# Kernel optimization log

Hardware: AMD Instinct MI355X
Metric: run time of the kernel (lower is better)

Reference implementation:

```python
import jax, jax.numpy as jnp
import numpy as np
from functools import partial

B, T, F, H = 32768, 48, 16, 32  # batch, horizon, feature dim, rnn_size


def setup_inputs() -> dict:
    key = jax.random.key(0)
    ks = jax.random.split(key, 9)
    return {
        "decoder_feature": jax.random.normal(ks[0], (B, T, F), dtype=jnp.float32),
        "decoder_init_input": jax.random.normal(ks[1], (B, 1), dtype=jnp.float32),
        "init_state": jax.random.normal(ks[2], (B, H), dtype=jnp.float32),
        # GRUCell (Keras default reset_after=True): kernel [in_dim, 3H], recurrent [H, 3H], two biases
        "kernel": jax.random.normal(ks[3], (1 + F, 3 * H), dtype=jnp.float32) * 0.1,
        "recurrent_kernel": jax.random.normal(ks[4], (H, 3 * H), dtype=jnp.float32) * 0.1,
        "bias_x": jax.random.normal(ks[5], (3 * H,), dtype=jnp.float32) * 0.1,
        "bias_h": jax.random.normal(ks[6], (3 * H,), dtype=jnp.float32) * 0.1,
        "dense_w": jax.random.normal(ks[7], (H, 1), dtype=jnp.float32) * 0.1,
        "dense_b": jax.random.normal(ks[8], (1,), dtype=jnp.float32) * 0.1,
    }


def reference(decoder_feature, decoder_init_input, init_state,
              kernel, recurrent_kernel, bias_x, bias_h, dense_w, dense_b):
    units = init_state.shape[-1]

    def step(carry, feat_t):
        h, prev_out = carry                              # h: [B,H], prev_out: [B,1]
        x = jnp.concatenate([prev_out, feat_t], axis=1)  # [B, 1+F]
        mx = x @ kernel + bias_x                         # [B, 3H]
        mh = h @ recurrent_kernel + bias_h               # [B, 3H] (reset_after=True)
        xz, xr, xh = jnp.split(mx, 3, axis=1)
        hz, hr, hh_in = jnp.split(mh, 3, axis=1)
        z = jax.nn.sigmoid(xz + hz)
        r = jax.nn.sigmoid(xr + hr)
        hh = jnp.tanh(xh + r * hh_in)
        h_new = z * h + (1.0 - z) * hh                   # GRU output == new state
        out = h_new @ dense_w + dense_b                  # Dense(1): [B,1]
        return (h_new, out), out

    feats = jnp.transpose(decoder_feature, (1, 0, 2))    # [T,B,F] time-major for scan
    _, outs = jax.lax.scan(step, (init_state, decoder_init_input), feats)
    return jnp.transpose(outs, (1, 0, 2))                # [B,T,1]
```

## Files before the change

kernel.cpp:

```cpp
#include <hip/hip_runtime.h>


typedef __attribute__((ext_vector_type(8))) short short8;
typedef __attribute__((ext_vector_type(4))) float f32x4;

constexpr int T_STEPS = 48;
constexpr int F_DIM   = 16;
constexpr int H_DIM   = 32;
constexpr int ROW_SH  = 40;
constexpr int H_BYTES = 16 * ROW_SH * 2;
constexpr int O_FLOATS = 16 * T_STEPS;
constexpr int WAVE_BYTES = H_BYTES + O_FLOATS * 4;

union S8 { short8 s; unsigned u[4]; };

__device__ __forceinline__ unsigned pk_bf16(float hi, float lo) {
    return __builtin_amdgcn_perm(__float_as_uint(hi) + 0x8000u,
                                 __float_as_uint(lo) + 0x8000u, 0x07060302u);
}
__device__ __forceinline__ short bf16s(float x) {
    return (short)((__float_as_uint(x) + 0x8000u) >> 16);
}
__device__ __forceinline__ float fsig(float x) {
    return __builtin_amdgcn_rcpf(1.0f + __expf(-x));
}
__device__ __forceinline__ float ftanh(float x) {
    return 1.0f - 2.0f * __builtin_amdgcn_rcpf(__expf(2.0f * x) + 1.0f);
}
#define MFMA(a, b, c) __builtin_amdgcn_mfma_f32_16x16x32_bf16(a, b, c, 0, 0, 0)
#define SWZ16(v) __int_as_float(__builtin_amdgcn_ds_swizzle(__float_as_int(v), 0x401F))

__global__ __launch_bounds__(256, 2)
void gru_mfma4(const float* __restrict__ feat,
               const float* __restrict__ init_in,
               const float* __restrict__ init_h,
               const float* __restrict__ Wk,
               const float* __restrict__ Rk,
               const float* __restrict__ bx,
               const float* __restrict__ bh,
               const float* __restrict__ dw,
               const float* __restrict__ db,
               float* __restrict__ out)
{
    __shared__ __align__(16) char lds[4 * WAVE_BYTES];
    const int lane = threadIdx.x & 63;
    const int wave = threadIdx.x >> 6;
    const int ln   = lane & 15;
    const int quad = lane >> 4;
    const int b0   = (blockIdx.x * 4 + wave) * 16;

    char*  my   = lds + wave * WAVE_BYTES;
    short* hsh  = (short*)my;
    float* obuf = (float*)(my + H_BYTES);
    unsigned* hw = (unsigned*)(hsh + ln * ROW_SH + quad * 4);
    const short8* hr = (const short8*)(hsh + ln * ROW_SH + quad * 8);
    const int bpa = (lane ^ 32) << 2;

    S8 Wf[6], Rf[6];
#pragma unroll
    for (int tn = 0; tn < 6; ++tn) {
#pragma unroll
        for (int j = 0; j < 8; ++j) {
            const int k = quad * 8 + j;
            const int n = tn * 16 + ln;
            const float wv = (k < 16) ? Wk[(size_t)(k + 1) * 96 + n] : 0.0f;
            Wf[tn].s[j] = bf16s(wv);
            Rf[tn].s[j] = bf16s(Rk[(size_t)k * 96 + n]);
        }
    }

    float bz8[8], br8[8], bxh8[8], bhh8[8], wz8[8], wr8[8], wh8[8], dw8[8];
#pragma unroll
    for (int tn = 0; tn < 2; ++tn)
#pragma unroll
        for (int i = 0; i < 4; ++i) {
            const int c = tn * 16 + quad * 4 + i;
            const int idx = tn * 4 + i;
            bz8[idx]  = bx[c] + bh[c];
            br8[idx]  = bx[32 + c] + bh[32 + c];
            bxh8[idx] = bx[64 + c];
            bhh8[idx] = bh[64 + c];
            wz8[idx]  = Wk[c];
            wr8[idx]  = Wk[32 + c];
            wh8[idx]  = Wk[64 + c];
            dw8[idx]  = dw[c];
        }
    const float dbs = db[0];

    float hc[8];
#pragma unroll
    for (int tn = 0; tn < 2; ++tn)
#pragma unroll
        for (int i = 0; i < 4; ++i)
            hc[tn * 4 + i] = init_h[(size_t)(b0 + ln) * H_DIM + tn * 16 + quad * 4 + i];
    S8 hB;
    {
        const float* hp = init_h + (size_t)(b0 + ln) * H_DIM + quad * 8;
        const f32x4 a = *(const f32x4*)hp;
        const f32x4 b = *(const f32x4*)(hp + 4);
        hB.u[0] = pk_bf16(a[1], a[0]); hB.u[1] = pk_bf16(a[3], a[2]);
        hB.u[2] = pk_bf16(b[1], b[0]); hB.u[3] = pk_bf16(b[3], b[2]);
    }
    float po = init_in[b0 + ln];

    const float* fqb = feat + (size_t)(b0 + ln) * (T_STEPS * F_DIM) + (quad & 1) * 8;
    f32x4 pa = *(const f32x4*)(fqb);
    f32x4 pb = *(const f32x4*)(fqb + 4);

    for (int t = 0; t < T_STEPS; ++t) {
        S8 xa;
        xa.u[0] = pk_bf16(pa[1], pa[0]); xa.u[1] = pk_bf16(pa[3], pa[2]);
        xa.u[2] = pk_bf16(pb[1], pb[0]); xa.u[3] = pk_bf16(pb[3], pb[2]);
        const unsigned zm = (quad < 2) ? 0xFFFFFFFFu : 0u;
        xa.u[0] &= zm; xa.u[1] &= zm; xa.u[2] &= zm; xa.u[3] &= zm;

        const int t1 = (t < T_STEPS - 1) ? t + 1 : T_STEPS - 1;
        pa = *(const f32x4*)(fqb + t1 * F_DIM);
        pb = *(const f32x4*)(fqb + t1 * F_DIM + 4);

        f32x4 aZ[2], aR[2], aXH[2], aHH[2];
#pragma unroll
        for (int tn = 0; tn < 2; ++tn)
#pragma unroll
            for (int i = 0; i < 4; ++i) {
                const int idx = tn * 4 + i;
                aZ[tn][i]  = fmaf(po, wz8[idx], bz8[idx]);
                aR[tn][i]  = fmaf(po, wr8[idx], br8[idx]);
                aXH[tn][i] = fmaf(po, wh8[idx], bxh8[idx]);
                aHH[tn][i] = bhh8[idx];
            }
#pragma unroll
        for (int tn = 0; tn < 2; ++tn) {
            aZ[tn]  = MFMA(Wf[tn].s,     xa.s, aZ[tn]);
            aZ[tn]  = MFMA(Rf[tn].s,     hB.s, aZ[tn]);
            aR[tn]  = MFMA(Wf[2 + tn].s, xa.s, aR[tn]);
            aR[tn]  = MFMA(Rf[2 + tn].s, hB.s, aR[tn]);
            aXH[tn] = MFMA(Wf[4 + tn].s, xa.s, aXH[tn]);
            aHH[tn] = MFMA(Rf[4 + tn].s, hB.s, aHH[tn]);
        }

        float hn[8];
        float partial = 0.0f;
#pragma unroll
        for (int tn = 0; tn < 2; ++tn)
#pragma unroll
            for (int i = 0; i < 4; ++i) {
                const int idx = tn * 4 + i;
                const float zz = fsig(aZ[tn][i]);
                const float rr = fsig(aR[tn][i]);
                const float cc = ftanh(aXH[tn][i] + rr * aHH[tn][i]);
                const float h2 = cc + zz * (hc[idx] - cc);
                hc[idx] = h2;
                hn[idx] = h2;
                partial = fmaf(h2, dw8[idx], partial);
            }

        float s1 = partial + SWZ16(partial);
        s1 += __int_as_float(__builtin_amdgcn_ds_bpermute(bpa, __float_as_int(s1)));
        const float o = s1 + dbs;
        if (quad == 0) obuf[t * 16 + ln] = o;
        po = o;

        hw[0] = pk_bf16(hn[1], hn[0]);
        hw[1] = pk_bf16(hn[3], hn[2]);
        hw[8] = pk_bf16(hn[5], hn[4]);
        hw[9] = pk_bf16(hn[7], hn[6]);
        hB.s = *hr;
    }

    const int row = lane >> 2;
    const int tb  = (lane & 3) * 12;
    float* orow = out + (size_t)(b0 + row) * T_STEPS + tb;
#pragma unroll
    for (int k = 0; k < 3; ++k) {
        f32x4 v;
#pragma unroll
        for (int e = 0; e < 4; ++e) v[e] = obuf[(tb + k * 4 + e) * 16 + row];
        *(f32x4*)(orow + k * 4) = v;
    }
}

extern "C" void kernel_launch(void* const* d_in, const int* in_sizes, int n_in,
                              void* d_out, int out_size, void* d_ws, size_t ws_size,
                              hipStream_t stream) {
    const float* feat    = (const float*)d_in[0];
    const float* init_in = (const float*)d_in[1];
    const float* init_h  = (const float*)d_in[2];
    const float* Wk      = (const float*)d_in[3];
    const float* Rk      = (const float*)d_in[4];
    const float* bx      = (const float*)d_in[5];
    const float* bh      = (const float*)d_in[6];
    const float* dw      = (const float*)d_in[7];
    const float* db      = (const float*)d_in[8];
    float* out           = (float*)d_out;

    const int B = in_sizes[2] / H_DIM;
    dim3 grid((unsigned)(B / 64));
    dim3 block(256);
    hipLaunchKernelGGL(gru_mfma4, grid, block, 0, stream,
                       feat, init_in, init_h, Wk, Rk, bx, bh, dw, db, out);
}
```

Baseline: 198.6 us.

## Redistribute hidden state via ds_bpermute instead of LDS round-trip, defer prev-output FMA

```diff
diff --git a/kernel.cpp b/kernel.cpp
--- a/kernel.cpp
+++ b/kernel.cpp
@@ -7,10 +7,8 @@
 constexpr int T_STEPS = 48;
 constexpr int F_DIM   = 16;
 constexpr int H_DIM   = 32;
-constexpr int ROW_SH  = 40;
-constexpr int H_BYTES = 16 * ROW_SH * 2;
-constexpr int O_FLOATS = 16 * T_STEPS;
-constexpr int WAVE_BYTES = H_BYTES + O_FLOATS * 4;
+constexpr int O_STRIDE = 17;
+constexpr int WAVE_FLOATS = T_STEPS * O_STRIDE;
 
 union S8 { short8 s; unsigned u[4]; };
 
@@ -29,9 +27,10 @@
 }
 #define MFMA(a, b, c) __builtin_amdgcn_mfma_f32_16x16x32_bf16(a, b, c, 0, 0, 0)
 #define SWZ16(v) __int_as_float(__builtin_amdgcn_ds_swizzle(__float_as_int(v), 0x401F))
+#define BPERM(a, v) __builtin_amdgcn_ds_bpermute((a), (v))
 
 __global__ __launch_bounds__(256, 2)
-void gru_mfma4(const float* __restrict__ feat,
+void gru_mfma5(const float* __restrict__ feat,
                const float* __restrict__ init_in,
                const float* __restrict__ init_h,
                const float* __restrict__ Wk,
@@ -42,19 +41,20 @@
                const float* __restrict__ db,
                float* __restrict__ out)
 {
-    __shared__ __align__(16) char lds[4 * WAVE_BYTES];
+    __shared__ __align__(16) float obufA[4 * WAVE_FLOATS];
     const int lane = threadIdx.x & 63;
     const int wave = threadIdx.x >> 6;
     const int ln   = lane & 15;
     const int quad = lane >> 4;
     const int b0   = (blockIdx.x * 4 + wave) * 16;
-
-    char*  my   = lds + wave * WAVE_BYTES;
-    short* hsh  = (short*)my;
-    float* obuf = (float*)(my + H_BYTES);
-    unsigned* hw = (unsigned*)(hsh + ln * ROW_SH + quad * 4);
-    const short8* hr = (const short8*)(hsh + ln * ROW_SH + quad * 8);
+    float* obuf = obufA + wave * WAVE_FLOATS;
+
+    const int s1  = ((quad & 1) << 1) | (quad >> 1);
+    const int aA  = (ln + 16 * s1) << 2;
+    const int aB  = aA ^ 64;
     const int bpa = (lane ^ 32) << 2;
+    const bool eodd = (quad & 1) != 0;
+    const bool lo2  = quad < 2;
 
     S8 Wf[6], Rf[6];
 #pragma unroll
@@ -111,7 +111,7 @@
         S8 xa;
         xa.u[0] = pk_bf16(pa[1], pa[0]); xa.u[1] = pk_bf16(pa[3], pa[2]);
         xa.u[2] = pk_bf16(pb[1], pb[0]); xa.u[3] = pk_bf16(pb[3], pb[2]);
-        const unsigned zm = (quad < 2) ? 0xFFFFFFFFu : 0u;
+        const unsigned zm = lo2 ? 0xFFFFFFFFu : 0u;
         xa.u[0] &= zm; xa.u[1] &= zm; xa.u[2] &= zm; xa.u[3] &= zm;
 
         const int t1 = (t < T_STEPS - 1) ? t + 1 : T_STEPS - 1;
@@ -123,49 +123,59 @@
         for (int tn = 0; tn < 2; ++tn)
 #pragma unroll
             for (int i = 0; i < 4; ++i) {
-                const int idx = tn * 4 + i;
-                aZ[tn][i]  = fmaf(po, wz8[idx], bz8[idx]);
-                aR[tn][i]  = fmaf(po, wr8[idx], br8[idx]);
-                aXH[tn][i] = fmaf(po, wh8[idx], bxh8[idx]);
-                aHH[tn][i] = bhh8[idx];
+                aZ[tn][i]  = bz8[tn * 4 + i];
+                aR[tn][i]  = br8[tn * 4 + i];
+                aXH[tn][i] = bxh8[tn * 4 + i];
+                aHH[tn][i] = bhh8[tn * 4 + i];
             }
 #pragma unroll
         for (int tn = 0; tn < 2; ++tn) {
             aZ[tn]  = MFMA(Wf[tn].s,     xa.s, aZ[tn]);
+            aR[tn]  = MFMA(Wf[2 + tn].s, xa.s, aR[tn]);
+            aXH[tn] = MFMA(Wf[4 + tn].s, xa.s, aXH[tn]);
             aZ[tn]  = MFMA(Rf[tn].s,     hB.s, aZ[tn]);
-            aR[tn]  = MFMA(Wf[2 + tn].s, xa.s, aR[tn]);
             aR[tn]  = MFMA(Rf[2 + tn].s, hB.s, aR[tn]);
-            aXH[tn] = MFMA(Wf[4 + tn].s, xa.s, aXH[tn]);
             aHH[tn] = MFMA(Rf[4 + tn].s, hB.s, aHH[tn]);
         }
 
         float hn[8];
-        float partial = 0.0f;
 #pragma unroll
         for (int tn = 0; tn < 2; ++tn)
 #pragma unroll
             for (int i = 0; i < 4; ++i) {
                 const int idx = tn * 4 + i;
-                const float zz = fsig(aZ[tn][i]);
-                const float rr = fsig(aR[tn][i]);
-                const float cc = ftanh(aXH[tn][i] + rr * aHH[tn][i]);
+                const float zz = fsig(fmaf(po, wz8[idx], aZ[tn][i]));
+                const float rr = fsig(fmaf(po, wr8[idx], aR[tn][i]));
+                const float cc = ftanh(fmaf(po, wh8[idx], aXH[tn][i]) + rr * aHH[tn][i]);
                 const float h2 = cc + zz * (hc[idx] - cc);
                 hc[idx] = h2;
                 hn[idx] = h2;
-                partial = fmaf(h2, dw8[idx], partial);
             }
 
-        float s1 = partial + SWZ16(partial);
-        s1 += __int_as_float(__builtin_amdgcn_ds_bpermute(bpa, __float_as_int(s1)));
-        const float o = s1 + dbs;
-        if (quad == 0) obuf[t * 16 + ln] = o;
+        const float d01 = fmaf(hn[0], dw8[0], hn[1] * dw8[1]);
+        const float d23 = fmaf(hn[2], dw8[2], hn[3] * dw8[3]);
+        const float d45 = fmaf(hn[4], dw8[4], hn[5] * dw8[5]);
+        const float d67 = fmaf(hn[6], dw8[6], hn[7] * dw8[7]);
+        float partial = (d01 + d23) + (d45 + d67);
+
+        const unsigned p01 = pk_bf16(hn[1], hn[0]);
+        const unsigned p23 = pk_bf16(hn[3], hn[2]);
+        const unsigned p45 = pk_bf16(hn[5], hn[4]);
+        const unsigned p67 = pk_bf16(hn[7], hn[6]);
+        const unsigned b1 = (unsigned)BPERM(aA, (int)(eodd ? p45 : p01));
+        const unsigned b2 = (unsigned)BPERM(aA, (int)(eodd ? p67 : p23));
+        const unsigned b3 = (unsigned)BPERM(aB, (int)(eodd ? p01 : p45));
+        const unsigned b4 = (unsigned)BPERM(aB, (int)(eodd ? p23 : p67));
+        hB.u[0] = lo2 ? b1 : b3;
+        hB.u[1] = lo2 ? b2 : b4;
+        hB.u[2] = lo2 ? b3 : b1;
+        hB.u[3] = lo2 ? b4 : b2;
+
+        float s = partial + SWZ16(partial);
+        s += __int_as_float(BPERM(bpa, __float_as_int(s)));
+        const float o = s + dbs;
+        if (quad == 0) obuf[t * O_STRIDE + ln] = o;
         po = o;
-
-        hw[0] = pk_bf16(hn[1], hn[0]);
-        hw[1] = pk_bf16(hn[3], hn[2]);
-        hw[8] = pk_bf16(hn[5], hn[4]);
-        hw[9] = pk_bf16(hn[7], hn[6]);
-        hB.s = *hr;
     }
 
     const int row = lane >> 2;
@@ -175,7 +185,7 @@
     for (int k = 0; k < 3; ++k) {
         f32x4 v;
 #pragma unroll
-        for (int e = 0; e < 4; ++e) v[e] = obuf[(tb + k * 4 + e) * 16 + row];
+        for (int e2 = 0; e2 < 4; ++e2) v[e2] = obuf[(tb + k * 4 + e2) * O_STRIDE + row];
         *(f32x4*)(orow + k * 4) = v;
     }
 }
@@ -197,6 +207,6 @@
     const int B = in_sizes[2] / H_DIM;
     dim3 grid((unsigned)(B / 64));
     dim3 block(256);
-    hipLaunchKernelGGL(gru_mfma4, grid, block, 0, stream,
+    hipLaunchKernelGGL(gru_mfma5, grid, block, 0, stream,
                        feat, init_in, init_h, Wk, Rk, bx, bh, dw, db, out);
 }
```

Measured after the change: 196.5 us. About the same (-1.0%).

## Split hidden units of each 16-row tile across two waves with barrier exchange

Applied to the files above, without the earlier changes.

```diff
diff --git a/kernel.cpp b/kernel.cpp
--- a/kernel.cpp
+++ b/kernel.cpp
@@ -4,13 +4,12 @@
 typedef __attribute__((ext_vector_type(8))) short short8;
 typedef __attribute__((ext_vector_type(4))) float f32x4;
 
-constexpr int T_STEPS = 48;
-constexpr int F_DIM   = 16;
-constexpr int H_DIM   = 32;
-constexpr int ROW_SH  = 40;
-constexpr int H_BYTES = 16 * ROW_SH * 2;
-constexpr int O_FLOATS = 16 * T_STEPS;
-constexpr int WAVE_BYTES = H_BYTES + O_FLOATS * 4;
+constexpr int T_STEPS  = 48;
+constexpr int F_DIM    = 16;
+constexpr int H_DIM    = 32;
+constexpr int ROW_SH   = 40;
+constexpr int HX_SH    = 16 * ROW_SH;
+constexpr int O_STRIDE = 17;
 
 union S8 { short8 s; unsigned u[4]; };
 
@@ -21,17 +20,14 @@
 __device__ __forceinline__ short bf16s(float x) {
     return (short)((__float_as_uint(x) + 0x8000u) >> 16);
 }
-__device__ __forceinline__ float fsig(float x) {
-    return __builtin_amdgcn_rcpf(1.0f + __expf(-x));
-}
-__device__ __forceinline__ float ftanh(float x) {
-    return 1.0f - 2.0f * __builtin_amdgcn_rcpf(__expf(2.0f * x) + 1.0f);
-}
+__device__ __forceinline__ float rcpf(float x) { return __builtin_amdgcn_rcpf(x); }
+__device__ __forceinline__ float ex2(float x)  { return __builtin_amdgcn_exp2f(x); }
 #define MFMA(a, b, c) __builtin_amdgcn_mfma_f32_16x16x32_bf16(a, b, c, 0, 0, 0)
 #define SWZ16(v) __int_as_float(__builtin_amdgcn_ds_swizzle(__float_as_int(v), 0x401F))
+#define BPERM(a, v) __builtin_amdgcn_ds_bpermute((a), (v))
 
-__global__ __launch_bounds__(256, 2)
-void gru_mfma4(const float* __restrict__ feat,
+__global__ __launch_bounds__(128, 4)
+void gru_mfma7(const float* __restrict__ feat,
                const float* __restrict__ init_in,
                const float* __restrict__ init_h,
                const float* __restrict__ Wk,
@@ -42,57 +38,53 @@
                const float* __restrict__ db,
                float* __restrict__ out)
 {
-    __shared__ __align__(16) char lds[4 * WAVE_BYTES];
+    __shared__ __align__(16) short hx[2 * HX_SH];
+    __shared__ float posum[2][2][16];
+    __shared__ __align__(16) float obuf[T_STEPS * O_STRIDE];
+
     const int lane = threadIdx.x & 63;
-    const int wave = threadIdx.x >> 6;
+    const int w    = threadIdx.x >> 6;
     const int ln   = lane & 15;
     const int quad = lane >> 4;
-    const int b0   = (blockIdx.x * 4 + wave) * 16;
+    const int b0   = blockIdx.x * 16;
+    const int bpa  = (lane ^ 32) << 2;
 
-    char*  my   = lds + wave * WAVE_BYTES;
-    short* hsh  = (short*)my;
-    float* obuf = (float*)(my + H_BYTES);
-    unsigned* hw = (unsigned*)(hsh + ln * ROW_SH + quad * 4);
-    const short8* hr = (const short8*)(hsh + ln * ROW_SH + quad * 8);
-    const int bpa = (lane ^ 32) << 2;
+    const float SZ = -1.44269504088896340736f;
+    const float SC =  2.88539008177792681472f;
 
-    S8 Wf[6], Rf[6];
+    S8 Wfz, Wfr, Wfh, Rfz, Rfr, Rfh;
 #pragma unroll
-    for (int tn = 0; tn < 6; ++tn) {
-#pragma unroll
-        for (int j = 0; j < 8; ++j) {
-            const int k = quad * 8 + j;
-            const int n = tn * 16 + ln;
-            const float wv = (k < 16) ? Wk[(size_t)(k + 1) * 96 + n] : 0.0f;
-            Wf[tn].s[j] = bf16s(wv);
-            Rf[tn].s[j] = bf16s(Rk[(size_t)k * 96 + n]);
-        }
+    for (int j = 0; j < 8; ++j) {
+        const int k = quad * 8 + j;
+        const int n = w * 16 + ln;
+        const float wz = (k < 16) ? SZ * Wk[(size_t)(k + 1) * 96 + n]      : 0.0f;
+        const float wr = (k < 16) ? SZ * Wk[(size_t)(k + 1) * 96 + 32 + n] : 0.0f;
+        const float wh = (k < 16) ? SC * Wk[(size_t)(k + 1) * 96 + 64 + n] : 0.0f;
+        Wfz.s[j] = bf16s(wz); Wfr.s[j] = bf16s(wr); Wfh.s[j] = bf16s(wh);
+        Rfz.s[j] = bf16s(SZ * Rk[(size_t)k * 96 + n]);
+        Rfr.s[j] = bf16s(SZ * Rk[(size_t)k * 96 + 32 + n]);
+        Rfh.s[j] = bf16s(SC * Rk[(size_t)k * 96 + 64 + n]);
     }
 
-    float bz8[8], br8[8], bxh8[8], bhh8[8], wz8[8], wr8[8], wh8[8], dw8[8];
+    float bz4[4], br4[4], bxh4[4], bhh4[4], wz4[4], wr4[4], wh4[4], dw4[4];
 #pragma unroll
-    for (int tn = 0; tn < 2; ++tn)
-#pragma unroll
-        for (int i = 0; i < 4; ++i) {
-            const int c = tn * 16 + quad * 4 + i;
-            const int idx = tn * 4 + i;
-            bz8[idx]  = bx[c] + bh[c];
-            br8[idx]  = bx[32 + c] + bh[32 + c];
-            bxh8[idx] = bx[64 + c];
-            bhh8[idx] = bh[64 + c];
-            wz8[idx]  = Wk[c];
-            wr8[idx]  = Wk[32 + c];
-            wh8[idx]  = Wk[64 + c];
-            dw8[idx]  = dw[c];
-        }
+    for (int i = 0; i < 4; ++i) {
+        const int c = w * 16 + quad * 4 + i;
+        bz4[i]  = SZ * (bx[c] + bh[c]);
+        br4[i]  = SZ * (bx[32 + c] + bh[32 + c]);
+        bxh4[i] = SC * bx[64 + c];
+        bhh4[i] = SC * bh[64 + c];
+        wz4[i]  = SZ * Wk[c];
+        wr4[i]  = SZ * Wk[32 + c];
+        wh4[i]  = SC * Wk[64 + c];
+        dw4[i]  = dw[c];
+    }
     const float dbs = db[0];
 
-    float hc[8];
+    float hc[4];
 #pragma unroll
-    for (int tn = 0; tn < 2; ++tn)
-#pragma unroll
-        for (int i = 0; i < 4; ++i)
-            hc[tn * 4 + i] = init_h[(size_t)(b0 + ln) * H_DIM + tn * 16 + quad * 4 + i];
+    for (int i = 0; i < 4; ++i)
+        hc[i] = init_h[(size_t)(b0 + ln) * H_DIM + w * 16 + quad * 4 + i];
     S8 hB;
     {
         const float* hp = init_h + (size_t)(b0 + ln) * H_DIM + quad * 8;
@@ -107,7 +99,12 @@
     f32x4 pa = *(const f32x4*)(fqb);
     f32x4 pb = *(const f32x4*)(fqb + 4);
 
+    unsigned* hwr = (unsigned*)(hx + ln * ROW_SH + w * 16 + quad * 4);
+    const short8* hrd = (const short8*)(hx + ln * ROW_SH + quad * 8);
+
     for (int t = 0; t < T_STEPS; ++t) {
+        const int p = t & 1;
+
         S8 xa;
         xa.u[0] = pk_bf16(pa[1], pa[0]); xa.u[1] = pk_bf16(pa[3], pa[2]);
         xa.u[2] = pk_bf16(pb[1], pb[0]); xa.u[3] = pk_bf16(pb[3], pb[2]);
@@ -118,65 +115,60 @@
         pa = *(const f32x4*)(fqb + t1 * F_DIM);
         pb = *(const f32x4*)(fqb + t1 * F_DIM + 4);
 
-        f32x4 aZ[2], aR[2], aXH[2], aHH[2];
+        f32x4 aZ  = {bz4[0],  bz4[1],  bz4[2],  bz4[3]};
+        f32x4 aR  = {br4[0],  br4[1],  br4[2],  br4[3]};
+        f32x4 aXH = {bxh4[0], bxh4[1], bxh4[2], bxh4[3]};
+        f32x4 aHH = {bhh4[0], bhh4[1], bhh4[2], bhh4[3]};
+        aZ  = MFMA(Wfz.s, xa.s, aZ);
+        aR  = MFMA(Wfr.s, xa.s, aR);
+        aXH = MFMA(Wfh.s, xa.s, aXH);
+        aZ  = MFMA(Rfz.s, hB.s, aZ);
+        aR  = MFMA(Rfr.s, hB.s, aR);
+        aHH = MFMA(Rfh.s, hB.s, aHH);
+
+        float hn[4];
 #pragma unroll
-        for (int tn = 0; tn < 2; ++tn)
-#pragma unroll
-            for (int i = 0; i < 4; ++i) {
-                const int idx = tn * 4 + i;
-                aZ[tn][i]  = fmaf(po, wz8[idx], bz8[idx]);
-                aR[tn][i]  = fmaf(po, wr8[idx], br8[idx]);
-                aXH[tn][i] = fmaf(po, wh8[idx], bxh8[idx]);
-                aHH[tn][i] = bhh8[idx];
-            }
-#pragma unroll
-        for (int tn = 0; tn < 2; ++tn) {
-            aZ[tn]  = MFMA(Wf[tn].s,     xa.s, aZ[tn]);
-            aZ[tn]  = MFMA(Rf[tn].s,     hB.s, aZ[tn]);
-            aR[tn]  = MFMA(Wf[2 + tn].s, xa.s, aR[tn]);
-            aR[tn]  = MFMA(Rf[2 + tn].s, hB.s, aR[tn]);
-            aXH[tn] = MFMA(Wf[4 + tn].s, xa.s, aXH[tn]);
-            aHH[tn] = MFMA(Rf[4 + tn].s, hB.s, aHH[tn]);
+        for (int i = 0; i < 4; ++i) {
+            const float zz = rcpf(1.0f + ex2(fmaf(po, wz4[i], aZ[i])));
+            const float rr = rcpf(1.0f + ex2(fmaf(po, wr4[i], aR[i])));
+            const float vv = fmaf(rr, aHH[i], fmaf(po, wh4[i], aXH[i]));
+            const float cc = fmaf(-2.0f, rcpf(1.0f + ex2(vv)), 1.0f);
+            const float h2 = cc + zz * (hc[i] - cc);
+            hc[i] = h2;
+            hn[i] = h2;
         }
 
-        float hn[8];
-        float partial = 0.0f;
-#pragma unroll
-        for (int tn = 0; tn < 2; ++tn)
-#pragma unroll
-            for (int i = 0; i < 4; ++i) {
-                const int idx = tn * 4 + i;
-                const float zz = fsig(aZ[tn][i]);
-                const float rr = fsig(aR[tn][i]);
-                const float cc = ftanh(aXH[tn][i] + rr * aHH[tn][i]);
-                const float h2 = cc + zz * (hc[idx] - cc);
-                hc[idx] = h2;
-                hn[idx] = h2;
-                partial = fmaf(h2, dw8[idx], partial);
-            }
+        const float d01 = fmaf(hn[0], dw4[0], hn[1] * dw4[1]);
+        const float d23 = fmaf(hn[2], dw4[2], hn[3] * dw4[3]);
+        float s = d01 + d23;
+        s += SWZ16(s);
+        s += __int_as_float(BPERM(bpa, __float_as_int(s)));
 
-        float s1 = partial + SWZ16(partial);
-        s1 += __int_as_float(__builtin_amdgcn_ds_bpermute(bpa, __float_as_int(s1)));
-        const float o = s1 + dbs;
-        if (quad == 0) obuf[t * 16 + ln] = o;
-        po = o;
-
+        unsigned* hw = hwr + p * (HX_SH / 2);
         hw[0] = pk_bf16(hn[1], hn[0]);
         hw[1] = pk_bf16(hn[3], hn[2]);
-        hw[8] = pk_bf16(hn[5], hn[4]);
-        hw[9] = pk_bf16(hn[7], hn[6]);
-        hB.s = *hr;
+        if (lane < 16) posum[p][w][lane] = s;
+
+        __builtin_amdgcn_s_waitcnt(0xC07F);
+        __builtin_amdgcn_s_barrier();
+
+        hB.s = hrd[p * (HX_SH / 8)];
+        const float os = posum[p][1 - w][ln];
+        po = s + os + dbs;
+        if (w == 0 && lane < 16) obuf[t * O_STRIDE + lane] = po;
     }
 
-    const int row = lane >> 2;
-    const int tb  = (lane & 3) * 12;
-    float* orow = out + (size_t)(b0 + row) * T_STEPS + tb;
+    if (w == 0) {
+        const int row = lane >> 2;
+        const int tb  = (lane & 3) * 12;
+        float* orow = out + (size_t)(b0 + row) * T_STEPS + tb;
 #pragma unroll
-    for (int k = 0; k < 3; ++k) {
-        f32x4 v;
+        for (int k = 0; k < 3; ++k) {
+            f32x4 v;
 #pragma unroll
-        for (int e = 0; e < 4; ++e) v[e] = obuf[(tb + k * 4 + e) * 16 + row];
-        *(f32x4*)(orow + k * 4) = v;
+            for (int e = 0; e < 4; ++e) v[e] = obuf[(tb + k * 4 + e) * O_STRIDE + row];
+            *(f32x4*)(orow + k * 4) = v;
+        }
     }
 }
 
@@ -195,8 +187,8 @@
     float* out           = (float*)d_out;
 
     const int B = in_sizes[2] / H_DIM;
-    dim3 grid((unsigned)(B / 64));
-    dim3 block(256);
-    hipLaunchKernelGGL(gru_mfma4, grid, block, 0, stream,
+    dim3 grid((unsigned)(B / 16));
+    dim3 block(128);
+    hipLaunchKernelGGL(gru_mfma7, grid, block, 0, stream,
                        feat, init_in, init_h, Wk, Rk, bx, bh, dw, db, out);
 }
```

Measured after the change: 193.3 us. 1.03x faster.
